# Optimization experiments

Hardware: AMD Instinct MI355X
Metric: run time of the kernel (lower is better)

## Reference

```python
import jax, jax.numpy as jnp
import numpy as np

EMBED = 192
EXPAND = 3
D1 = EMBED * EXPAND  # 576
RPE_IN = 32
LAYERS = 3
LAMBDA = 0.95


def _rpe_mlp(t, w0, b0, ws, bs, wo, bo):
    # t: (2n, 1) relative positions -> (2n, D1) Toeplitz coefficients
    h = t @ w0.T + b0
    for i in range(ws.shape[0]):
        h = jax.nn.relu(h) @ ws[i].T + bs[i]
    return jax.nn.relu(h) @ wo.T + bo


def _toeplitz(x, a):
    # Toeplitz matmul via length-2n circular convolution (FFT).
    # x: (B, n, d); a: (2n, d) coeffs ordered [t0, t1..t_{n-1}, pad, neg half]
    n = x.shape[1]
    m = 2 * n
    xf = jnp.fft.rfft(x, m, axis=1)
    af = jnp.fft.rfft(a, m, axis=0)
    return jnp.fft.irfft(xf * af[None], m, axis=1)[:, :n]


def _forward(x, p_w, p_b, q_w, q_b, v_w, v_b, o_w, o_b, slope,
             t1_w0, t1_b0, t1_ws, t1_bs, t1_wo, t1_bo,
             t2_w0, t2_b0, t2_ws, t2_bs, t2_wo, t2_bo):
    b, h, w, d = x.shape
    n = h  # square grid: h == w, rpe/decay built from n = x.shape[1]
    dt = x.dtype

    pos = jnp.arange(1, n, dtype=dt).reshape(-1, 1)          # (n-1, 1)
    zero = jnp.zeros((1, 1), dt)
    rpe_input = jnp.concatenate([zero, pos, zero, -pos], axis=0)  # (2n, 1)

    p = jax.nn.silu(x @ p_w.T + p_b)
    q = jax.nn.silu(x @ q_w.T + q_b)
    v = jax.nn.silu(x @ v_w.T + v_b)

    # decay mask: slope clamped to [0,1], blended with lambda, powered by |lag|
    sl = LAMBDA + (1.0 - LAMBDA) * jnp.clip(slope, 0.0, 1.0)  # (1, D1)
    idx = jnp.arange(1, n, dtype=dt).reshape(1, -1, 1)        # (1, n-1, 1)
    gamma = sl ** idx                                          # (1, n-1, D1)
    one = jnp.ones((1, 1, D1), dt)
    decay = jnp.concatenate([one, gamma, one, gamma[:, ::-1]], axis=1)[0]  # (2n, D1)

    a1 = _rpe_mlp(rpe_input, t1_w0, t1_b0, t1_ws, t1_bs, t1_wo, t1_bo) * decay
    a2 = _rpe_mlp(rpe_input, t2_w0, t2_b0, t2_ws, t2_bs, t2_wo, t2_bo) * decay

    qv = q * v                                                 # (b, h, w, D1)
    # axial mixing: tno1 along width, tno2 along height
    o1 = _toeplitz(qv.reshape(b * h, w, D1), a1).reshape(b, h, w, D1)
    o2 = _toeplitz(jnp.transpose(qv, (0, 2, 1, 3)).reshape(b * w, h, D1), a2)
    o2 = jnp.transpose(o2.reshape(b, w, h, D1), (0, 2, 1, 3))
    out = p * (o1 + o2)
    return out @ o_w.T + o_b


def setup_inputs() -> dict:
    key = jax.random.key(0)
    ks = jax.random.split(key, 8)

    def lin(k, out_d, in_d):
        k1, k2 = jax.random.split(k)
        s = 1.0 / np.sqrt(in_d)
        return (jax.random.uniform(k1, (out_d, in_d), jnp.float32, -s, s),
                jax.random.uniform(k2, (out_d,), jnp.float32, -s, s))

    x = jax.random.normal(ks[0], (8, 56, 56, EMBED), jnp.float32)
    p_w, p_b = lin(ks[1], D1, EMBED)
    q_w, q_b = lin(ks[2], D1, EMBED)
    v_w, v_b = lin(ks[3], D1, EMBED)
    o_w, o_b = lin(ks[4], EMBED, D1)
    # slope init: 1/arange(1, d1+1)^(1/(index+1)), index=0
    slope = (1.0 / jnp.arange(1, D1 + 1, dtype=jnp.float32)).reshape(1, -1)

    def tno_params(kb):
        kk = jax.random.split(kb, 2 + LAYERS)
        w0, b0 = lin(kk[0], RPE_IN, 1)
        ws, bs = [], []
        for i in range(LAYERS):
            wi, bi = lin(kk[1 + i], RPE_IN, RPE_IN)
            ws.append(wi); bs.append(bi)
        wo, bo = lin(kk[1 + LAYERS], D1, RPE_IN)
        return w0, b0, jnp.stack(ws), jnp.stack(bs), wo, bo

    t1 = tno_params(ks[5])
    t2 = tno_params(ks[6])
    return {"x": x, "p_w": p_w, "p_b": p_b, "q_w": q_w, "q_b": q_b,
            "v_w": v_w, "v_b": v_b, "o_w": o_w, "o_b": o_b, "slope": slope,
            "t1_w0": t1[0], "t1_b0": t1[1], "t1_ws": t1[2], "t1_bs": t1[3], "t1_wo": t1[4], "t1_bo": t1[5],
            "t2_w0": t2[0], "t2_b0": t2[1], "t2_ws": t2[2], "t2_bs": t2[3], "t2_wo": t2[4], "t2_bo": t2[5]}


def reference(x, p_w, p_b, q_w, q_b, v_w, v_b, o_w, o_b, slope,
              t1_w0, t1_b0, t1_ws, t1_bs, t1_wo, t1_bo,
              t2_w0, t2_b0, t2_ws, t2_bs, t2_wo, t2_bo):
    return _forward(x, p_w, p_b, q_w, q_b, v_w, v_b, o_w, o_b, slope,
                    t1_w0, t1_b0, t1_ws, t1_bs, t1_wo, t1_bo,
                    t2_w0, t2_b0, t2_ws, t2_bs, t2_wo, t2_bo)
```

## Files before the change

kernel.cpp:

```cpp
#include <hip/hip_runtime.h>
#include <hip/hip_bf16.h>
#include <math.h>

typedef unsigned short u16;
typedef short bf16x8 __attribute__((ext_vector_type(8)));
typedef float f32x4 __attribute__((ext_vector_type(4)));

#define NB 8
#define NN 56
#define M2 112
#define EMB 192
#define D1 576
#define TOK (NB*NN*NN)

__device__ __forceinline__ float bf2f(unsigned int u) {
    union { unsigned int i; float f; } v; v.i = u << 16; return v.f;
}
__device__ __forceinline__ u16 f2bf(float f) {
    union { float f; unsigned int i; } v; v.f = f;
    unsigned int x = v.i;
    return (u16)((x + 0x7fffu + ((x >> 16) & 1u)) >> 16);
}
__device__ __forceinline__ float silu(float x) {
    return x / (1.0f + __expf(-x));
}
__device__ __forceinline__ void async16(void* lds, const void* g) {
    __builtin_amdgcn_global_load_lds(
        (const __attribute__((address_space(1))) void*)g,
        (__attribute__((address_space(3))) void*)lds, 16, 0, 0);
}

#define XCH (TOK*EMB/4)
#define WCH (D1*EMB/4)
__global__ __launch_bounds__(256) void convert_kernel(
    const float* __restrict__ x,
    const float* __restrict__ pw, const float* __restrict__ qw,
    const float* __restrict__ vw, const float* __restrict__ ow,
    u16* __restrict__ xb, u16* __restrict__ wb, u16* __restrict__ owb)
{
    int tid = blockIdx.x * 256 + threadIdx.x;
    const float* src; u16* dst; int off;
    if (tid < XCH) { src = x; dst = xb; off = tid; }
    else {
        int r = tid - XCH;
        int seg = r / WCH; off = r % WCH;
        if (seg == 0)      { src = pw; dst = wb; }
        else if (seg == 1) { src = qw; dst = wb + D1*EMB; }
        else if (seg == 2) { src = vw; dst = wb + 2*D1*EMB; }
        else if (seg == 3) { src = ow; dst = owb; }
        else return;
    }
    float4 f = *(const float4*)(src + off * 4);
    ushort4 o;
    o.x = f2bf(f.x); o.y = f2bf(f.y); o.z = f2bf(f.z); o.w = f2bf(f.w);
    *(ushort4*)(dst + off * 4) = o;
}

__global__ __launch_bounds__(576) void rpe_kernel(
    const float* __restrict__ slope,
    const float* w0a, const float* b0a, const float* wsa, const float* bsa,
    const float* woa, const float* boa,
    const float* w0b, const float* b0b, const float* wsb, const float* bsb,
    const float* wob, const float* bob,
    float* __restrict__ A1, float* __restrict__ A2)
{
    int wq  = blockIdx.x / M2;
    int row = blockIdx.x % M2;
    const float* w0 = wq ? w0b : w0a;  const float* b0 = wq ? b0b : b0a;
    const float* ws = wq ? wsb : wsa;  const float* bs = wq ? bsb : bsa;
    const float* wo = wq ? wob : woa;  const float* bo = wq ? bob : boa;
    float* A = wq ? A2 : A1;

    float tval = (row == 0 || row == 56) ? 0.0f
               : (row < 56 ? (float)row : -(float)(row - 56));
    int kexp = (row == 0 || row == 56) ? 0 : (row < 56 ? row : 112 - row);

    __shared__ float h[32], g[32];
    int t = threadIdx.x;
    if (t < 32) h[t] = tval * w0[t] + b0[t];
    __syncthreads();
    for (int L = 0; L < 3; L++) {
        if (t < 32) g[t] = fmaxf(h[t], 0.0f);
        __syncthreads();
        float hn = 0.0f;
        if (t < 32) {
            hn = bs[L * 32 + t];
            for (int k = 0; k < 32; k++)
                hn = fmaf(g[k], ws[(L * 32 + t) * 32 + k], hn);
        }
        __syncthreads();
        if (t < 32) h[t] = hn;
        __syncthreads();
    }
    if (t < 32) g[t] = fmaxf(h[t], 0.0f);
    __syncthreads();

    float o = bo[t];
    for (int k = 0; k < 32; k++)
        o = fmaf(g[k], wo[t * 32 + k], o);

    float sl = slope[t];
    sl = 0.95f + 0.05f * fminf(fmaxf(sl, 0.0f), 1.0f);
    float dec = powf(sl, (float)kexp);
    A[row * D1 + t] = o * dec;
}

__global__ __launch_bounds__(256) void tbuild_kernel(
    const float* __restrict__ A1, const float* __restrict__ A2,
    u16* __restrict__ T1t, u16* __restrict__ T2t)
{
    int d = blockIdx.x;
    const float* src = blockIdx.y ? A2 : A1;
    u16* dst = blockIdx.y ? T2t : T1t;
    __shared__ float win[111];
    int t = threadIdx.x;
    if (t < 111) {
        int lag = t - 55;
        int rowi = lag + (lag < 0 ? 112 : 0);
        win[t] = src[rowi * D1 + d];
    }
    __syncthreads();
    int i = t >> 2, jq = (t & 3) * 16;
    u16 vals[16];
    #pragma unroll
    for (int jj = 0; jj < 16; jj++) {
        int j = jq + jj;
        float v = (i < 56 && j < 56) ? win[i - j + 55] : 0.0f;
        vals[jj] = f2bf(v);
    }
    u16* out = dst + ((size_t)d * 64 + i) * 64 + jq;
    *(uint4*)(out)     = *(uint4*)&vals[0];
    *(uint4*)(out + 8) = *(uint4*)&vals[8];
}

__global__ __launch_bounds__(256) void proj_kernel(
    const u16* __restrict__ xb, const u16* __restrict__ wb,
    const float* __restrict__ pb, const float* __restrict__ qb,
    const float* __restrict__ vb,
    u16* __restrict__ P_T, u16* __restrict__ QV_T)
{
    __shared__ u16 lds[20480];
    u16* As = lds;
    u16* Bs = lds + 8192;
    int m0 = blockIdx.x * 128, n0 = blockIdx.y * 64;
    int t = threadIdx.x;
    int l = t & 63, wave = t >> 6;
    int wm = wave >> 1, wn = wave & 1;
    int col16 = l & 15, q = l >> 4;

    f32x4 accp[4][2], accq[4][2], accv[4][2];
    #pragma unroll
    for (int i = 0; i < 4; i++)
        #pragma unroll
        for (int j = 0; j < 2; j++) {
            accp[i][j] = (f32x4){0,0,0,0};
            accq[i][j] = (f32x4){0,0,0,0};
            accv[i][j] = (f32x4){0,0,0,0};
        }

    for (int k0 = 0; k0 < EMB; k0 += 64) {
        #pragma unroll
        for (int ii = 0; ii < 4; ii++) {
            int slot = (ii * 4 + wave) * 64 + l;
            int r = slot >> 3, s = slot & 7;
            int g = s ^ (r & 7);
            async16(&As[slot * 8], xb + (m0 + r) * EMB + k0 + g * 8);
        }
        #pragma unroll
        for (int ii = 0; ii < 6; ii++) {
            int slot = (ii * 4 + wave) * 64 + l;
            int mat = slot >> 9, cc = slot & 511;
            int r = cc >> 3, s = cc & 7;
            int g = s ^ (r & 7);
            async16(&Bs[slot * 8],
                    wb + mat * (D1 * EMB) + (n0 + r) * EMB + k0 + g * 8);
        }
        __syncthreads();

        #pragma unroll
        for (int kk = 0; kk < 2; kk++) {
            bf16x8 af[4];
            #pragma unroll
            for (int mt = 0; mt < 4; mt++) {
                int row = wm * 64 + mt * 16 + col16;
                int sw = (q + 4 * kk) ^ (col16 & 7);
                af[mt] = *(const bf16x8*)&As[row * 64 + sw * 8];
            }
            bf16x8 bfr[3][2];
            #pragma unroll
            for (int mat = 0; mat < 3; mat++)
                #pragma unroll
                for (int nt = 0; nt < 2; nt++) {
                    int row = wn * 32 + nt * 16 + col16;
                    int sw = (q + 4 * kk) ^ (col16 & 7);
                    bfr[mat][nt] = *(const bf16x8*)&Bs[mat * 4096 + row * 64 + sw * 8];
                }
            #pragma unroll
            for (int mt = 0; mt < 4; mt++)
                #pragma unroll
                for (int nt = 0; nt < 2; nt++) {
                    accp[mt][nt] = __builtin_amdgcn_mfma_f32_16x16x32_bf16(
                        af[mt], bfr[0][nt], accp[mt][nt], 0, 0, 0);
                    accq[mt][nt] = __builtin_amdgcn_mfma_f32_16x16x32_bf16(
                        af[mt], bfr[1][nt], accq[mt][nt], 0, 0, 0);
                    accv[mt][nt] = __builtin_amdgcn_mfma_f32_16x16x32_bf16(
                        af[mt], bfr[2][nt], accv[mt][nt], 0, 0, 0);
                }
        }
        __syncthreads();
    }

    u16* scr = lds + wave * 2688;
    float pbv[2], qbv[2], vbv[2];
    #pragma unroll
    for (int nt = 0; nt < 2; nt++) {
        int n = n0 + wn * 32 + nt * 16 + col16;
        pbv[nt] = pb[n]; qbv[nt] = qb[n]; vbv[nt] = vb[n];
    }
    #pragma unroll
    for (int mt = 0; mt < 4; mt++)
        #pragma unroll
        for (int nt = 0; nt < 2; nt++)
            #pragma unroll
            for (int r = 0; r < 4; r++)
                scr[(mt * 16 + q * 4 + r) * 42 + nt * 16 + col16] =
                    f2bf(silu(accp[mt][nt][r] + pbv[nt]));
    #pragma unroll
    for (int dl = 0; dl < 32; dl++)
        P_T[(size_t)(n0 + wn * 32 + dl) * TOK + m0 + wm * 64 + l] =
            scr[l * 42 + dl];
    #pragma unroll
    for (int mt = 0; mt < 4; mt++)
        #pragma unroll
        for (int nt = 0; nt < 2; nt++)
            #pragma unroll
            for (int r = 0; r < 4; r++)
                scr[(mt * 16 + q * 4 + r) * 42 + nt * 16 + col16] =
                    f2bf(silu(accq[mt][nt][r] + qbv[nt]) *
                         silu(accv[mt][nt][r] + vbv[nt]));
    #pragma unroll
    for (int dl = 0; dl < 32; dl++)
        QV_T[(size_t)(n0 + wn * 32 + dl) * TOK + m0 + wm * 64 + l] =
            scr[l * 42 + dl];
}

__global__ __launch_bounds__(256) void tno_mfma(
    const u16* __restrict__ QV_T, const u16* __restrict__ T1t,
    const u16* __restrict__ T2t, const u16* __restrict__ P_T,
    u16* __restrict__ U_T)
{
    __shared__ u16 T1s[4096];
    __shared__ u16 T2s[4096];
    __shared__ u16 Qn[64 * 72];
    __shared__ u16 Qt[64 * 72];
    __shared__ float O1f[56 * 68];
    int d = blockIdx.x, b = blockIdx.y;
    int t = threadIdx.x;
    size_t base = (size_t)d * TOK + (size_t)b * 3136;

    #pragma unroll
    for (int k = 0; k < 2; k++) {
        int slot = t + k * 256;
        int i = slot >> 3, s = slot & 7;
        int g = s ^ (i & 7);
        async16(&T1s[slot * 8], T1t + ((size_t)d * 64 + i) * 64 + g * 8);
        async16(&T2s[slot * 8], T2t + ((size_t)d * 64 + i) * 64 + g * 8);
    }
    for (int c = t; c < 392; c += 256) {
        int h = c / 7, w8 = (c % 7) * 8;
        uint4 v = *(const uint4*)(QV_T + base + c * 8);
        *(uint4*)&Qn[h * 72 + w8] = v;
        u16 e[8];
        *(uint4*)e = v;
        #pragma unroll
        for (int k = 0; k < 8; k++)
            Qt[(w8 + k) * 72 + h] = e[k];
    }
    if (t < 56) {
        uint4 z = {0, 0, 0, 0};
        *(uint4*)&Qn[t * 72 + 56] = z;
        *(uint4*)&Qt[t * 72 + 56] = z;
    }
    __syncthreads();

    int l = t & 63, wave = t >> 6;
    int col16 = l & 15, q = l >> 4;

    f32x4 acc1[4], acc2[4];
    #pragma unroll
    for (int i = 0; i < 4; i++) { acc1[i] = (f32x4){0,0,0,0}; acc2[i] = (f32x4){0,0,0,0}; }

    #pragma unroll
    for (int kk = 0; kk < 2; kk++) {
        int sw = ((q + 4 * kk) ^ (col16 & 7)) * 8;
        bf16x8 bq1 = *(const bf16x8*)&Qn[(wave * 16 + col16) * 72 + kk * 32 + q * 8];
        bf16x8 bq2 = *(const bf16x8*)&Qt[(wave * 16 + col16) * 72 + kk * 32 + q * 8];
        #pragma unroll
        for (int mt = 0; mt < 4; mt++) {
            bf16x8 a1 = *(const bf16x8*)&T1s[(mt * 16 + col16) * 64 + sw];
            bf16x8 a2 = *(const bf16x8*)&T2s[(mt * 16 + col16) * 64 + sw];
            acc1[mt] = __builtin_amdgcn_mfma_f32_16x16x32_bf16(a1, bq1, acc1[mt], 0, 0, 0);
            acc2[mt] = __builtin_amdgcn_mfma_f32_16x16x32_bf16(a2, bq2, acc2[mt], 0, 0, 0);
        }
    }

    {
        int n = wave * 16 + col16;
        if (n < 56) {
            #pragma unroll
            for (int mt = 0; mt < 4; mt++)
                #pragma unroll
                for (int r = 0; r < 4; r++) {
                    int m = mt * 16 + q * 4 + r;
                    if (m < 56) O1f[n * 68 + m] = acc1[mt][r];
                }
        }
    }
    __syncthreads();
    {
        int n = wave * 16 + col16;
        if (n < 56) {
            #pragma unroll
            for (int mt = 0; mt < 4; mt++)
                #pragma unroll
                for (int r = 0; r < 4; r++) {
                    int m = mt * 16 + q * 4 + r;
                    if (m < 56) O1f[m * 68 + n] += acc2[mt][r];
                }
        }
    }
    __syncthreads();
    for (int c = t; c < 392; c += 256) {
        int h = c / 7, w8 = (c % 7) * 8;
        f32x4 s0 = *(const f32x4*)&O1f[h * 68 + w8];
        f32x4 s1 = *(const f32x4*)&O1f[h * 68 + w8 + 4];
        uint4 pv = *(const uint4*)(P_T + base + c * 8);
        u16 pe[8];
        *(uint4*)pe = pv;
        u16 ue[8];
        #pragma unroll
        for (int k = 0; k < 4; k++) ue[k] = f2bf(bf2f(pe[k]) * s0[k]);
        #pragma unroll
        for (int k = 0; k < 4; k++) ue[4 + k] = f2bf(bf2f(pe[4 + k]) * s1[k]);
        *(uint4*)(U_T + base + c * 8) = *(uint4*)ue;
    }
}

__global__ __launch_bounds__(256) void transp_kernel(
    const u16* __restrict__ U_T, u16* __restrict__ U)
{
    __shared__ u16 tile[64 * 72];
    int t = threadIdx.x;
    int t0 = blockIdx.x * 64;
    int d0 = blockIdx.y * 64;
    {
        int dr = t >> 2, c = t & 3;
        #pragma unroll
        for (int h = 0; h < 2; h++) {
            int cc = c + h * 4;
            uint4 v = *(const uint4*)(U_T + (size_t)(d0 + dr) * TOK + t0 + cc * 8);
            *(uint4*)&tile[dr * 72 + cc * 8] = v;
        }
    }
    __syncthreads();
    {
        int tr = t & 63, c4 = t >> 6;
        u16 vals[16];
        #pragma unroll
        for (int k = 0; k < 16; k++)
            vals[k] = tile[(c4 * 16 + k) * 72 + tr];
        u16* dst = U + (size_t)(t0 + tr) * D1 + d0 + c4 * 16;
        *(uint4*)(dst)     = *(uint4*)&vals[0];
        *(uint4*)(dst + 8) = *(uint4*)&vals[8];
    }
}

__global__ __launch_bounds__(256) void outproj_kernel(
    const u16* __restrict__ U, const u16* __restrict__ owb,
    const float* __restrict__ ob, float* __restrict__ out)
{
    __shared__ char ldsraw[36864];
    u16* As = (u16*)ldsraw;
    u16* Bs = (u16*)(ldsraw + 16384);
    int m0 = blockIdx.x * 128, n0 = blockIdx.y * 64;
    int t = threadIdx.x;
    int l = t & 63, wave = t >> 6;
    int wm = wave >> 1, wn = wave & 1;
    int col16 = l & 15, q = l >> 4;

    f32x4 acc[4][2];
    #pragma unroll
    for (int i = 0; i < 4; i++)
        #pragma unroll
        for (int j = 0; j < 2; j++) acc[i][j] = (f32x4){0,0,0,0};

    for (int k0 = 0; k0 < D1; k0 += 64) {
        #pragma unroll
        for (int ii = 0; ii < 4; ii++) {
            int slot = (ii * 4 + wave) * 64 + l;
            int r = slot >> 3, s = slot & 7;
            int g = s ^ (r & 7);
            async16(&As[slot * 8], U + (m0 + r) * D1 + k0 + g * 8);
        }
        #pragma unroll
        for (int ii = 0; ii < 2; ii++) {
            int slot = (ii * 4 + wave) * 64 + l;
            int r = slot >> 3, s = slot & 7;
            int g = s ^ (r & 7);
            async16(&Bs[slot * 8], owb + (n0 + r) * D1 + k0 + g * 8);
        }
        __syncthreads();

        #pragma unroll
        for (int kk = 0; kk < 2; kk++) {
            int sw = (q + 4 * kk) ^ (col16 & 7);
            bf16x8 af[4];
            #pragma unroll
            for (int mt = 0; mt < 4; mt++)
                af[mt] = *(const bf16x8*)&As[(wm * 64 + mt * 16 + col16) * 64 + sw * 8];
            bf16x8 bfr[2];
            #pragma unroll
            for (int nt = 0; nt < 2; nt++)
                bfr[nt] = *(const bf16x8*)&Bs[(wn * 32 + nt * 16 + col16) * 64 + sw * 8];
            #pragma unroll
            for (int mt = 0; mt < 4; mt++)
                #pragma unroll
                for (int nt = 0; nt < 2; nt++)
                    acc[mt][nt] = __builtin_amdgcn_mfma_f32_16x16x32_bf16(
                        af[mt], bfr[nt], acc[mt][nt], 0, 0, 0);
        }
        __syncthreads();
    }

    float* scr = (float*)ldsraw + wave * 2304;
    float obv[2];
    #pragma unroll
    for (int nt = 0; nt < 2; nt++)
        obv[nt] = ob[n0 + wn * 32 + nt * 16 + col16];
    #pragma unroll
    for (int mt = 0; mt < 4; mt++)
        #pragma unroll
        for (int nt = 0; nt < 2; nt++)
            #pragma unroll
            for (int r = 0; r < 4; r++)
                scr[(mt * 16 + q * 4 + r) * 36 + nt * 16 + col16] =
                    acc[mt][nt][r] + obv[nt];
    #pragma unroll
    for (int k = 0; k < 8; k++) {
        int row = k * 8 + (l >> 3), cs = (l & 7) * 4;
        f32x4 v = *(const f32x4*)&scr[row * 36 + cs];
        *(f32x4*)&out[(m0 + wm * 64 + row) * EMB + n0 + wn * 32 + cs] = v;
    }
}

extern "C" void kernel_launch(void* const* d_in, const int* in_sizes, int n_in,
                              void* d_out, int out_size, void* d_ws, size_t ws_size,
                              hipStream_t stream)
{
    (void)in_sizes; (void)n_in; (void)out_size; (void)ws_size;
    const float* x     = (const float*)d_in[0];
    const float* p_w   = (const float*)d_in[1];
    const float* p_b   = (const float*)d_in[2];
    const float* q_w   = (const float*)d_in[3];
    const float* q_b   = (const float*)d_in[4];
    const float* v_w   = (const float*)d_in[5];
    const float* v_b   = (const float*)d_in[6];
    const float* o_w   = (const float*)d_in[7];
    const float* o_b   = (const float*)d_in[8];
    const float* slope = (const float*)d_in[9];
    const float* t1_w0 = (const float*)d_in[10];
    const float* t1_b0 = (const float*)d_in[11];
    const float* t1_ws = (const float*)d_in[12];
    const float* t1_bs = (const float*)d_in[13];
    const float* t1_wo = (const float*)d_in[14];
    const float* t1_bo = (const float*)d_in[15];
    const float* t2_w0 = (const float*)d_in[16];
    const float* t2_b0 = (const float*)d_in[17];
    const float* t2_ws = (const float*)d_in[18];
    const float* t2_bs = (const float*)d_in[19];
    const float* t2_wo = (const float*)d_in[20];
    const float* t2_bo = (const float*)d_in[21];

    char* ws = (char*)d_ws;
    float* A1  = (float*)ws;
    float* A2  = (float*)(ws + 258048);
    u16*   PU  = (u16*)(ws + 516096);
    u16*   QVT = (u16*)(ws + 29417472);
    u16*   UT  = (u16*)(ws + 58318848);
    u16*   xb  = (u16*)(ws + 87220224);
    u16*   wb  = (u16*)(ws + 96854016);
    u16*   owb = (u16*)(ws + 97517568);
    u16*   T1t = (u16*)(ws + 97738752);
    u16*   T2t = (u16*)(ws + 102457344);

    convert_kernel<<<(XCH + 4*WCH + 255) / 256, 256, 0, stream>>>(
        x, p_w, q_w, v_w, o_w, xb, wb, owb);
    rpe_kernel<<<224, 576, 0, stream>>>(slope,
        t1_w0, t1_b0, t1_ws, t1_bs, t1_wo, t1_bo,
        t2_w0, t2_b0, t2_ws, t2_bs, t2_wo, t2_bo, A1, A2);
    tbuild_kernel<<<dim3(576, 2), 256, 0, stream>>>(A1, A2, T1t, T2t);
    proj_kernel<<<dim3(TOK / 128, D1 / 64), 256, 0, stream>>>(
        xb, wb, p_b, q_b, v_b, PU, QVT);
    tno_mfma<<<dim3(D1, NB), 256, 0, stream>>>(QVT, T1t, T2t, PU, UT);
    transp_kernel<<<dim3(TOK / 64, D1 / 64), 256, 0, stream>>>(UT, PU);
    outproj_kernel<<<dim3(TOK / 128, EMB / 64), 256, 0, stream>>>(
        PU, owb, o_b, (float*)d_out);
}
```

Before: 220.4 us.

## Double-buffer projection GEMM LDS staging and pack transposed epilogue stores

Splits the projection kernel's shared memory into two stage buffers, so the async global-to-LDS load of the next K chunk is issued while MFMAs run on the current chunk, overlapping load latency with compute. It also rewrites the transposed P and QV epilogue so each lane writes two adjacent bf16 tokens as one 32-bit store instead of single 16-bit stores. The cost is doubled LDS per block (80 KB), which may cut blocks per CU, and correctness depends on the loop-end barrier also waiting for the outstanding async copies.

```diff
diff --git a/kernel.cpp b/kernel.cpp
--- a/kernel.cpp
+++ b/kernel.cpp
@@ -139,9 +139,7 @@
     const float* __restrict__ vb,
     u16* __restrict__ P_T, u16* __restrict__ QV_T)
 {
-    __shared__ u16 lds[20480];
-    u16* As = lds;
-    u16* Bs = lds + 8192;
+    __shared__ u16 lds[40960];
     int m0 = blockIdx.x * 128, n0 = blockIdx.y * 64;
     int t = threadIdx.x;
     int l = t & 63, wave = t >> 6;
@@ -158,13 +156,14 @@
             accv[i][j] = (f32x4){0,0,0,0};
         }
 
-    for (int k0 = 0; k0 < EMB; k0 += 64) {
+    auto stage = [&](int kc, int buf) {
+        int bo = buf * 20480;
         #pragma unroll
         for (int ii = 0; ii < 4; ii++) {
             int slot = (ii * 4 + wave) * 64 + l;
             int r = slot >> 3, s = slot & 7;
             int g = s ^ (r & 7);
-            async16(&As[slot * 8], xb + (m0 + r) * EMB + k0 + g * 8);
+            async16(&lds[bo + slot * 8], xb + (m0 + r) * EMB + kc * 64 + g * 8);
         }
         #pragma unroll
         for (int ii = 0; ii < 6; ii++) {
@@ -172,11 +171,19 @@
             int mat = slot >> 9, cc = slot & 511;
             int r = cc >> 3, s = cc & 7;
             int g = s ^ (r & 7);
-            async16(&Bs[slot * 8],
-                    wb + mat * (D1 * EMB) + (n0 + r) * EMB + k0 + g * 8);
-        }
-        __syncthreads();
-
+            async16(&lds[bo + 8192 + slot * 8],
+                    wb + mat * (D1 * EMB) + (n0 + r) * EMB + kc * 64 + g * 8);
+        }
+    };
+
+    stage(0, 0);
+    __syncthreads();
+
+    #pragma unroll
+    for (int kc = 0; kc < 3; kc++) {
+        int buf = kc & 1;
+        if (kc < 2) stage(kc + 1, buf ^ 1);
+        int bo = buf * 20480;
         #pragma unroll
         for (int kk = 0; kk < 2; kk++) {
             bf16x8 af[4];
@@ -184,7 +191,7 @@
             for (int mt = 0; mt < 4; mt++) {
                 int row = wm * 64 + mt * 16 + col16;
                 int sw = (q + 4 * kk) ^ (col16 & 7);
-                af[mt] = *(const bf16x8*)&As[row * 64 + sw * 8];
+                af[mt] = *(const bf16x8*)&lds[bo + row * 64 + sw * 8];
             }
             bf16x8 bfr[3][2];
             #pragma unroll
@@ -193,7 +200,7 @@
                 for (int nt = 0; nt < 2; nt++) {
                     int row = wn * 32 + nt * 16 + col16;
                     int sw = (q + 4 * kk) ^ (col16 & 7);
-                    bfr[mat][nt] = *(const bf16x8*)&Bs[mat * 4096 + row * 64 + sw * 8];
+                    bfr[mat][nt] = *(const bf16x8*)&lds[bo + 8192 + mat * 4096 + row * 64 + sw * 8];
                 }
             #pragma unroll
             for (int mt = 0; mt < 4; mt++)
@@ -217,6 +224,8 @@
         int n = n0 + wn * 32 + nt * 16 + col16;
         pbv[nt] = pb[n]; qbv[nt] = qb[n]; vbv[nt] = vb[n];
     }
+    int tok = (l & 31) * 2;
+    int dh = l >> 5;
     #pragma unroll
     for (int mt = 0; mt < 4; mt++)
         #pragma unroll
@@ -226,9 +235,12 @@
                 scr[(mt * 16 + q * 4 + r) * 42 + nt * 16 + col16] =
                     f2bf(silu(accp[mt][nt][r] + pbv[nt]));
     #pragma unroll
-    for (int dl = 0; dl < 32; dl++)
-        P_T[(size_t)(n0 + wn * 32 + dl) * TOK + m0 + wm * 64 + l] =
-            scr[l * 42 + dl];
+    for (int i = 0; i < 16; i++) {
+        int dl = i * 2 + dh;
+        unsigned int v = (unsigned int)scr[tok * 42 + dl] |
+                         ((unsigned int)scr[(tok + 1) * 42 + dl] << 16);
+        *(unsigned int*)&P_T[(size_t)(n0 + wn * 32 + dl) * TOK + m0 + wm * 64 + tok] = v;
+    }
     #pragma unroll
     for (int mt = 0; mt < 4; mt++)
         #pragma unroll
@@ -239,9 +251,12 @@
                     f2bf(silu(accq[mt][nt][r] + qbv[nt]) *
                          silu(accv[mt][nt][r] + vbv[nt]));
     #pragma unroll
-    for (int dl = 0; dl < 32; dl++)
-        QV_T[(size_t)(n0 + wn * 32 + dl) * TOK + m0 + wm * 64 + l] =
-            scr[l * 42 + dl];
+    for (int i = 0; i < 16; i++) {
+        int dl = i * 2 + dh;
+        unsigned int v = (unsigned int)scr[tok * 42 + dl] |
+                         ((unsigned int)scr[(tok + 1) * 42 + dl] << 16);
+        *(unsigned int*)&QV_T[(size_t)(n0 + wn * 32 + dl) * TOK + m0 + wm * 64 + tok] = v;
+    }
 }
 
 __global__ __launch_bounds__(256) void tno_mfma(
```

After: 224.1 us. About the same (+1.6%).
